# Kernel tuning notes

Measured on AMD Instinct MI355X. Metric: run time of the kernel, lower is better.

The kernel has to match this reference:

```python
import jax, jax.numpy as jnp
import numpy as np

D_MODEL = 1024
N_HEADS = 16
D_HEAD = D_MODEL // N_HEADS
WINDOW = 64
SCALE = 1.0 / np.sqrt(D_HEAD)


def setup_inputs() -> dict:
    key = jax.random.key(0)
    k1, k2, k3 = jax.random.split(key, 3)
    B, N = 1, 4096
    x = jax.random.normal(k1, (B, N, D_MODEL), dtype=jnp.float32)
    # xavier-uniform-ish init for weights (scaled normal is fine for a numeric reference)
    w_qkv = jax.random.normal(k2, (3 * D_MODEL, D_MODEL), dtype=jnp.float32) * (1.0 / np.sqrt(D_MODEL))
    b_qkv = jnp.zeros((3 * D_MODEL,), dtype=jnp.float32)
    w_out = jax.random.normal(k3, (D_MODEL, D_MODEL), dtype=jnp.float32) * (1.0 / np.sqrt(D_MODEL))
    b_out = jnp.zeros((D_MODEL,), dtype=jnp.float32)
    return {"x": x, "w_qkv": w_qkv, "b_qkv": b_qkv, "w_out": w_out, "b_out": b_out}


def reference(x, w_qkv, b_qkv, w_out, b_out):
    B, N, D = x.shape
    # QKV projection (torch Linear: x @ W^T + b)
    qkv = x @ w_qkv.T + b_qkv                      # [B, N, 3D]
    qkv = qkv.reshape(B, N, 3, N_HEADS, D_HEAD)
    qkv = jnp.transpose(qkv, (2, 0, 3, 1, 4))       # [3, B, H, N, dh]
    q, k, v = qkv[0], qkv[1], qkv[2]
    # dense scores, masked to causal sliding window (faithful to original)
    scores = jnp.einsum('bhqd,bhkd->bhqk', q, k) * SCALE  # [B, H, N, N]
    qpos = jnp.arange(N)[:, None]
    kpos = jnp.arange(N)[None, :]
    diff = qpos - kpos
    mask = (diff >= 0) & (diff < WINDOW)            # [N, N]
    scores = jnp.where(mask[None, None, :, :], scores, -jnp.inf)
    attn = jax.nn.softmax(scores, axis=-1)          # every query has >=1 valid key (self)
    out = jnp.einsum('bhqk,bhkd->bhqd', attn, v)    # [B, H, N, dh]
    out = jnp.transpose(out, (0, 2, 1, 3)).reshape(B, N, D)
    out = out @ w_out.T + b_out
    return out
```

## Files before the change

### kernel.cpp

```cpp
#include <hip/hip_runtime.h>
#include <hip/hip_bf16.h>
#include <stdint.h>
#include <stddef.h>

#define NSEQ  4096
#define DM    1024
#define NHEAD 16
#define DHEAD 64
#define WIN   64

using short8 = __attribute__((ext_vector_type(8))) short;
using f32x4  = __attribute__((ext_vector_type(4))) float;

#define GLOBAL_AS __attribute__((address_space(1)))
#define LDS_AS    __attribute__((address_space(3)))

__device__ __forceinline__ unsigned short f2bf(float f) {
  union { float f; unsigned int u; } v; v.f = f;
  unsigned int r = v.u + 0x7FFFu + ((v.u >> 16) & 1u);
  return (unsigned short)(r >> 16);
}

__device__ __forceinline__ void gload_lds16(void* lds, const void* g) {
  __builtin_amdgcn_global_load_lds((const GLOBAL_AS unsigned int*)g,
                                   (LDS_AS unsigned int*)lds, 16, 0, 0);
}

__global__ void cvt_kernel(const float* __restrict__ src,
                           unsigned short* __restrict__ dst, int n4) {
  int i = blockIdx.x * blockDim.x + threadIdx.x;
  if (i < n4) {
    float4 f = ((const float4*)src)[i];
    ushort4 o;
    o.x = f2bf(f.x); o.y = f2bf(f.y); o.z = f2bf(f.z); o.w = f2bf(f.w);
    ((ushort4*)dst)[i] = o;
  }
}

template<int EPI>
__global__ __launch_bounds__(256)
void gemm_bt(const unsigned short* __restrict__ A,
             const unsigned short* __restrict__ B,
             const float* __restrict__ bias,
             float* __restrict__ Cf,
             unsigned short* __restrict__ qo,
             unsigned short* __restrict__ ko,
             unsigned short* __restrict__ vo,
             int M, int N, int K) {
  __shared__ short As[2][128 * 32];
  __shared__ short Bs[2][128 * 32];

  const int nbn = N >> 7;
  const int bm  = blockIdx.x / nbn;
  const int bn  = blockIdx.x % nbn;
  const int tid = threadIdx.x;
  const int w   = tid >> 6;
  const int l   = tid & 63;
  const int wr  = w >> 1, wc = w & 1;
  const int l15 = l & 15, l4 = l >> 4;

  const int m0 = bm << 7;
  const int n0 = bn << 7;

  f32x4 acc[4][4] = {};

  const int nkt = K >> 5;

  auto stage = [&](int buf, int kt) {
    const int kbase = kt << 5;
#pragma unroll
    for (int r = 0; r < 2; ++r) {
      const int c   = r * 4 + w;
      const int row = c * 16 + (l >> 2);
      const int ke  = (l & 3) << 3;
      gload_lds16(&As[buf][c * 512 + l * 8],
                  A + (size_t)(m0 + row) * K + kbase + ke);
      gload_lds16(&Bs[buf][c * 512 + l * 8],
                  B + (size_t)(n0 + row) * K + kbase + ke);
    }
  };

  stage(0, 0);
  int cur = 0;
  for (int kt = 0; kt < nkt; ++kt) {
    __syncthreads();
    if (kt + 1 < nkt) stage(cur ^ 1, kt + 1);
    short8 a[4], b[4];
#pragma unroll
    for (int mi = 0; mi < 4; ++mi)
      a[mi] = *(const short8*)&As[cur][(wr * 64 + mi * 16 + l15) * 32 + l4 * 8];
#pragma unroll
    for (int ni = 0; ni < 4; ++ni)
      b[ni] = *(const short8*)&Bs[cur][(wc * 64 + ni * 16 + l15) * 32 + l4 * 8];
#pragma unroll
    for (int mi = 0; mi < 4; ++mi)
#pragma unroll
      for (int ni = 0; ni < 4; ++ni)
        acc[mi][ni] = __builtin_amdgcn_mfma_f32_16x16x32_bf16(a[mi], b[ni], acc[mi][ni], 0, 0, 0);
    cur ^= 1;
  }

  if (EPI == 0) {
#pragma unroll
    for (int ni = 0; ni < 4; ++ni) {
      const int n  = n0 + wc * 64 + ni * 16 + l15;
      const float bv = bias[n];
      const int region = n >> 10;
#pragma unroll
      for (int mi = 0; mi < 4; ++mi) {
        const int mb = m0 + wr * 64 + mi * 16 + l4 * 4;
        if (region == 0) {
          const int h = (n >> 6) & 15, d = n & 63;
#pragma unroll
          for (int r = 0; r < 4; ++r)
            qo[((size_t)(h * NSEQ + mb + r)) * DHEAD + d] =
                f2bf((acc[mi][ni][r] + bv) * 0.125f);
        } else if (region == 1) {
          const int nn = n - 1024;
          const int h = nn >> 6, d = nn & 63;
#pragma unroll
          for (int r = 0; r < 4; ++r)
            ko[((size_t)(h * NSEQ + mb + r)) * DHEAD + d] =
                f2bf(acc[mi][ni][r] + bv);
        } else {
          const int nn = n - 2048;
          ushort4 pk;
          pk.x = f2bf(acc[mi][ni][0] + bv);
          pk.y = f2bf(acc[mi][ni][1] + bv);
          pk.z = f2bf(acc[mi][ni][2] + bv);
          pk.w = f2bf(acc[mi][ni][3] + bv);
          *(ushort4*)&vo[(size_t)nn * NSEQ + mb] = pk;
        }
      }
    }
  } else {
#pragma unroll
    for (int ni = 0; ni < 4; ++ni) {
      const int n  = n0 + wc * 64 + ni * 16 + l15;
      const float bv = bias[n];
#pragma unroll
      for (int mi = 0; mi < 4; ++mi) {
        const int mb = m0 + wr * 64 + mi * 16 + l4 * 4;
#pragma unroll
        for (int r = 0; r < 4; ++r)
          Cf[(size_t)(mb + r) * N + n] = acc[mi][ni][r] + bv;
      }
    }
  }
}

__global__ __launch_bounds__(256)
void attn_kernel(const unsigned short* __restrict__ Qb,
                 const unsigned short* __restrict__ Kb,
                 const unsigned short* __restrict__ Vt,
                 unsigned short* __restrict__ att) {
  __shared__ short Pl[4][16][136];
  const int h  = blockIdx.x >> 6;
  const int q0 = (blockIdx.x & 63) << 6;
  const int w  = threadIdx.x >> 6;
  const int l  = threadIdx.x & 63;
  const int l15 = l & 15, l4 = l >> 4;
  const int qw = q0 + w * 16;

  const unsigned short* Qh = Qb + (size_t)h * NSEQ * DHEAD;
  const unsigned short* Kh = Kb + (size_t)h * NSEQ * DHEAD;
  const unsigned short* Vh = Vt + (size_t)h * DHEAD * NSEQ;

  short8 aq[2];
  {
    const int qrow = qw + l15;
    aq[0] = *(const short8*)&Qh[(size_t)qrow * DHEAD + l4 * 8];
    aq[1] = *(const short8*)&Qh[(size_t)qrow * DHEAD + 32 + l4 * 8];
  }

  f32x4 s[8] = {};
#pragma unroll
  for (int t = 0; t < 8; ++t) {
    int j  = q0 - 64 + t * 16 + l15;
    int jc = j < 0 ? 0 : j;
    short8 b0 = *(const short8*)&Kh[(size_t)jc * DHEAD + l4 * 8];
    short8 b1 = *(const short8*)&Kh[(size_t)jc * DHEAD + 32 + l4 * 8];
    s[t] = __builtin_amdgcn_mfma_f32_16x16x32_bf16(aq[0], b0, s[t], 0, 0, 0);
    s[t] = __builtin_amdgcn_mfma_f32_16x16x32_bf16(aq[1], b1, s[t], 0, 0, 0);
  }

  float rmax[4] = {-3e38f, -3e38f, -3e38f, -3e38f};
#pragma unroll
  for (int t = 0; t < 8; ++t)
#pragma unroll
    for (int r = 0; r < 4; ++r) {
      const int i = qw + l4 * 4 + r;
      const int j = q0 - 64 + t * 16 + l15;
      const int diff = i - j;
      float sv = (j >= 0 && diff >= 0 && diff < WIN) ? s[t][r] : -3e38f;
      s[t][r] = sv;
      rmax[r] = fmaxf(rmax[r], sv);
    }
#pragma unroll
  for (int r = 0; r < 4; ++r)
#pragma unroll
    for (int m = 1; m < 16; m <<= 1)
      rmax[r] = fmaxf(rmax[r], __shfl_xor(rmax[r], m, 64));

  float rsum[4] = {0.f, 0.f, 0.f, 0.f};
#pragma unroll
  for (int t = 0; t < 8; ++t)
#pragma unroll
    for (int r = 0; r < 4; ++r) {
      float p = __expf(s[t][r] - rmax[r]);
      s[t][r] = p;
      rsum[r] += p;
    }
#pragma unroll
  for (int r = 0; r < 4; ++r)
#pragma unroll
    for (int m = 1; m < 16; m <<= 1)
      rsum[r] += __shfl_xor(rsum[r], m, 64);

#pragma unroll
  for (int t = 0; t < 8; ++t)
#pragma unroll
    for (int r = 0; r < 4; ++r)
      Pl[w][l4 * 4 + r][t * 16 + l15] = (short)f2bf(s[t][r]);

  f32x4 o[4] = {};
#pragma unroll
  for (int ks = 0; ks < 4; ++ks) {
    short8 ap = *(const short8*)&Pl[w][l15][ks * 32 + l4 * 8];
    int jg = q0 - 64 + ks * 32 + l4 * 8;
    if (jg < 0) jg = 0;
#pragma unroll
    for (int dt = 0; dt < 4; ++dt) {
      const int d = dt * 16 + l15;
      short8 bv = *(const short8*)&Vh[(size_t)d * NSEQ + jg];
      o[dt] = __builtin_amdgcn_mfma_f32_16x16x32_bf16(ap, bv, o[dt], 0, 0, 0);
    }
  }

#pragma unroll
  for (int r = 0; r < 4; ++r) {
    const float rinv = 1.0f / rsum[r];
    const int m = qw + l4 * 4 + r;
#pragma unroll
    for (int dt = 0; dt < 4; ++dt)
      att[(size_t)m * DM + h * DHEAD + dt * 16 + l15] = f2bf(o[dt][r] * rinv);
  }
}

extern "C" void kernel_launch(void* const* d_in, const int* in_sizes, int n_in,
                              void* d_out, int out_size, void* d_ws, size_t ws_size,
                              hipStream_t stream) {
  const float* x    = (const float*)d_in[0];
  const float* wqkv = (const float*)d_in[1];
  const float* bqkv = (const float*)d_in[2];
  const float* wout = (const float*)d_in[3];
  const float* bout = (const float*)d_in[4];
  float* out = (float*)d_out;

  unsigned short* ws = (unsigned short*)d_ws;
  unsigned short* xb    = ws;
  unsigned short* wqkvb = xb    + (size_t)NSEQ * DM;
  unsigned short* woutb = wqkvb + (size_t)3 * DM * DM;
  unsigned short* qb    = woutb + (size_t)DM * DM;
  unsigned short* kb    = qb    + (size_t)NSEQ * DM;
  unsigned short* vtb   = kb    + (size_t)NSEQ * DM;
  unsigned short* attb  = vtb   + (size_t)NSEQ * DM;

  cvt_kernel<<<(NSEQ * DM / 4 + 255) / 256, 256, 0, stream>>>(x, xb, NSEQ * DM / 4);
  cvt_kernel<<<(3 * DM * DM / 4 + 255) / 256, 256, 0, stream>>>(wqkv, wqkvb, 3 * DM * DM / 4);
  cvt_kernel<<<(DM * DM / 4 + 255) / 256, 256, 0, stream>>>(wout, woutb, DM * DM / 4);

  gemm_bt<0><<<(NSEQ / 128) * (3 * DM / 128), 256, 0, stream>>>(
      xb, wqkvb, bqkv, nullptr, qb, kb, vtb, NSEQ, 3 * DM, DM);

  attn_kernel<<<NHEAD * (NSEQ / 64), 256, 0, stream>>>(qb, kb, vtb, attb);

  gemm_bt<1><<<(NSEQ / 128) * (DM / 128), 256, 0, stream>>>(
      attb, woutb, bout, out, nullptr, nullptr, nullptr, NSEQ, DM, DM);
}
```

Before: 98.05 us.

## Replace QKV projection GEMM with 256x256-tile 8-wave triple-buffered kernel

Adds a dedicated QKV projection kernel using 256x256 output tiles, 512 threads (8 waves), a three-stage LDS ring buffer with XOR-swizzled layout, explicit vmcnt waits and barriers, and setprio around the MFMA blocks. The larger tile gives more reuse per loaded byte, and the deeper pipeline overlaps global-to-LDS loads with compute. The trade-off is that the grid shrinks to 192 blocks, fewer than the number of CUs, and register pressure rises with 32 accumulators per lane. The generic GEMM template is reduced to the output-projection path only.

```diff
diff --git a/kernel.cpp b/kernel.cpp
--- a/kernel.cpp
+++ b/kernel.cpp
@@ -8,6 +8,7 @@
 #define NHEAD 16
 #define DHEAD 64
 #define WIN   64
+#define K_QKV 1024
 
 using short8 = __attribute__((ext_vector_type(8))) short;
 using f32x4  = __attribute__((ext_vector_type(4))) float;
@@ -37,15 +38,123 @@
   }
 }
 
-template<int EPI>
+__global__ __launch_bounds__(512, 2)
+void gemm_qkv8(const unsigned short* __restrict__ A,
+               const unsigned short* __restrict__ B,
+               const float* __restrict__ bias,
+               unsigned short* __restrict__ qo,
+               unsigned short* __restrict__ ko,
+               unsigned short* __restrict__ vo) {
+  __shared__ short lds[12 * 4096];
+
+  const int bm = blockIdx.x / 12;
+  const int bn = blockIdx.x % 12;
+  const int m0 = bm << 8, n0 = bn << 8;
+  const int tid = threadIdx.x, w = tid >> 6, l = tid & 63;
+  const int wr = w >> 2, wc = w & 3;
+  const int l15 = l & 15, l4 = l >> 4;
+
+  const int srow = (w << 4) + (l >> 2);
+  const int skel = ((l & 3) << 3) ^ ((l >= 32) << 4);
+  const int sdst = (w << 9) + (l << 3);
+
+  f32x4 acc[8][4] = {};
+
+  auto stage = [&](int s, int slot) {
+    const int h = s & 3, t = s >> 2;
+    const unsigned short* src;
+    if (h < 2) src = A + (size_t)(m0 + (h << 7) + srow) * K_QKV + (t << 5) + skel;
+    else       src = B + (size_t)(n0 + ((h & 1) << 7) + srow) * K_QKV + (t << 5) + skel;
+    gload_lds16(&lds[slot * 4096 + sdst], src);
+  };
+
+#pragma unroll
+  for (int s = 0; s < 8; ++s) stage(s, s);
+  asm volatile("s_waitcnt vmcnt(4)" ::: "memory");
+  asm volatile("s_barrier" ::: "memory");
+
+  const int NT = K_QKV / 32;
+  int bufC = 0;
+  for (int t = 0; t < NT; ++t) {
+    const int sbase = 4 * t + 8;
+    const int slotb = (bufC == 0 ? 2 : bufC - 1) * 4;
+    const short* At = &lds[(bufC * 4 + wr) * 4096];
+    const short* Bt = &lds[(bufC * 4 + 2 + (wc >> 1)) * 4096];
+    const int bn0 = (wc & 1) << 6;
+    short8 af[4], bf[2];
+#pragma unroll
+    for (int q = 0; q < 4; ++q) {
+      const int qa = q >> 1, qb = q & 1;
+      if (qb == 0) {
+#pragma unroll
+        for (int mi = 0; mi < 4; ++mi) {
+          const int sr = qa * 4 + mi;
+          af[mi] = *(const short8*)&At[sr * 512 + l15 * 32 + ((l4 * 8) ^ ((l15 >= 8) * 16))];
+        }
+      }
+#pragma unroll
+      for (int ni = 0; ni < 2; ++ni) {
+        const int sr = (bn0 >> 4) + qb * 2 + ni;
+        bf[ni] = *(const short8*)&Bt[sr * 512 + l15 * 32 + ((l4 * 8) ^ ((l15 >= 8) * 16))];
+      }
+      if (t < NT - 2) stage(sbase + q, slotb + q);
+      if (q == 3) {
+        if (t < NT - 2)      asm volatile("s_waitcnt vmcnt(4)" ::: "memory");
+        else if (t == NT - 2) asm volatile("s_waitcnt vmcnt(0)" ::: "memory");
+      }
+      asm volatile("s_barrier" ::: "memory");
+      __builtin_amdgcn_s_setprio(1);
+#pragma unroll
+      for (int mi = 0; mi < 4; ++mi)
+#pragma unroll
+        for (int ni = 0; ni < 2; ++ni)
+          acc[qa * 4 + mi][qb * 2 + ni] = __builtin_amdgcn_mfma_f32_16x16x32_bf16(
+              af[mi], bf[ni], acc[qa * 4 + mi][qb * 2 + ni], 0, 0, 0);
+      __builtin_amdgcn_s_setprio(0);
+      asm volatile("s_barrier" ::: "memory");
+    }
+    bufC = bufC == 2 ? 0 : bufC + 1;
+  }
+
+#pragma unroll
+  for (int ni = 0; ni < 4; ++ni) {
+    const int gn = n0 + wc * 64 + ni * 16 + l15;
+    const float bv = bias[gn];
+    const int region = gn >> 10;
+#pragma unroll
+    for (int mi = 0; mi < 8; ++mi) {
+      const int gm = m0 + wr * 128 + mi * 16 + l4 * 4;
+      if (region == 0) {
+        const int h = (gn >> 6) & 15, d = gn & 63;
+#pragma unroll
+        for (int r = 0; r < 4; ++r)
+          qo[((size_t)(h * NSEQ + gm + r)) * DHEAD + d] =
+              f2bf((acc[mi][ni][r] + bv) * 0.125f);
+      } else if (region == 1) {
+        const int nn = gn - 1024;
+        const int h = nn >> 6, d = nn & 63;
+#pragma unroll
+        for (int r = 0; r < 4; ++r)
+          ko[((size_t)(h * NSEQ + gm + r)) * DHEAD + d] =
+              f2bf(acc[mi][ni][r] + bv);
+      } else {
+        const int nn = gn - 2048;
+        ushort4 pk;
+        pk.x = f2bf(acc[mi][ni][0] + bv);
+        pk.y = f2bf(acc[mi][ni][1] + bv);
+        pk.z = f2bf(acc[mi][ni][2] + bv);
+        pk.w = f2bf(acc[mi][ni][3] + bv);
+        *(ushort4*)&vo[(size_t)nn * NSEQ + gm] = pk;
+      }
+    }
+  }
+}
+
 __global__ __launch_bounds__(256)
 void gemm_bt(const unsigned short* __restrict__ A,
              const unsigned short* __restrict__ B,
              const float* __restrict__ bias,
              float* __restrict__ Cf,
-             unsigned short* __restrict__ qo,
-             unsigned short* __restrict__ ko,
-             unsigned short* __restrict__ vo,
              int M, int N, int K) {
   __shared__ short As[2][128 * 32];
   __shared__ short Bs[2][128 * 32];
@@ -63,7 +172,6 @@
   const int n0 = bn << 7;
 
   f32x4 acc[4][4] = {};
-
   const int nkt = K >> 5;
 
   auto stage = [&](int buf, int kt) {
@@ -100,51 +208,16 @@
     cur ^= 1;
   }
 
-  if (EPI == 0) {
-#pragma unroll
-    for (int ni = 0; ni < 4; ++ni) {
-      const int n  = n0 + wc * 64 + ni * 16 + l15;
-      const float bv = bias[n];
-      const int region = n >> 10;
-#pragma unroll
-      for (int mi = 0; mi < 4; ++mi) {
-        const int mb = m0 + wr * 64 + mi * 16 + l4 * 4;
-        if (region == 0) {
-          const int h = (n >> 6) & 15, d = n & 63;
-#pragma unroll
-          for (int r = 0; r < 4; ++r)
-            qo[((size_t)(h * NSEQ + mb + r)) * DHEAD + d] =
-                f2bf((acc[mi][ni][r] + bv) * 0.125f);
-        } else if (region == 1) {
-          const int nn = n - 1024;
-          const int h = nn >> 6, d = nn & 63;
-#pragma unroll
-          for (int r = 0; r < 4; ++r)
-            ko[((size_t)(h * NSEQ + mb + r)) * DHEAD + d] =
-                f2bf(acc[mi][ni][r] + bv);
-        } else {
-          const int nn = n - 2048;
-          ushort4 pk;
-          pk.x = f2bf(acc[mi][ni][0] + bv);
-          pk.y = f2bf(acc[mi][ni][1] + bv);
-          pk.z = f2bf(acc[mi][ni][2] + bv);
-          pk.w = f2bf(acc[mi][ni][3] + bv);
-          *(ushort4*)&vo[(size_t)nn * NSEQ + mb] = pk;
-        }
-      }
-    }
-  } else {
-#pragma unroll
-    for (int ni = 0; ni < 4; ++ni) {
-      const int n  = n0 + wc * 64 + ni * 16 + l15;
-      const float bv = bias[n];
-#pragma unroll
-      for (int mi = 0; mi < 4; ++mi) {
-        const int mb = m0 + wr * 64 + mi * 16 + l4 * 4;
-#pragma unroll
-        for (int r = 0; r < 4; ++r)
-          Cf[(size_t)(mb + r) * N + n] = acc[mi][ni][r] + bv;
-      }
+#pragma unroll
+  for (int ni = 0; ni < 4; ++ni) {
+    const int n  = n0 + wc * 64 + ni * 16 + l15;
+    const float bv = bias[n];
+#pragma unroll
+    for (int mi = 0; mi < 4; ++mi) {
+      const int mb = m0 + wr * 64 + mi * 16 + l4 * 4;
+#pragma unroll
+      for (int r = 0; r < 4; ++r)
+        Cf[(size_t)(mb + r) * N + n] = acc[mi][ni][r] + bv;
     }
   }
 }
@@ -270,11 +343,11 @@
   cvt_kernel<<<(3 * DM * DM / 4 + 255) / 256, 256, 0, stream>>>(wqkv, wqkvb, 3 * DM * DM / 4);
   cvt_kernel<<<(DM * DM / 4 + 255) / 256, 256, 0, stream>>>(wout, woutb, DM * DM / 4);
 
-  gemm_bt<0><<<(NSEQ / 128) * (3 * DM / 128), 256, 0, stream>>>(
-      xb, wqkvb, bqkv, nullptr, qb, kb, vtb, NSEQ, 3 * DM, DM);
+  gemm_qkv8<<<(NSEQ / 256) * (3 * DM / 256), 512, 0, stream>>>(
+      xb, wqkvb, bqkv, qb, kb, vtb);
 
   attn_kernel<<<NHEAD * (NSEQ / 64), 256, 0, stream>>>(qb, kb, vtb, attb);
 
-  gemm_bt<1><<<(NSEQ / 128) * (DM / 128), 256, 0, stream>>>(
-      attb, woutb, bout, out, nullptr, nullptr, nullptr, NSEQ, DM, DM);
-}
+  gemm_bt<<<(NSEQ / 128) * (DM / 128), 256, 0, stream>>>(
+      attb, woutb, bout, out, NSEQ, DM, DM);
+}
```

Result: slower. 101.0 us (+3.0%).

## Triple-buffer GEMM with swizzled LDS, fine-grained waitcnt, and fused conversion kernel

Applied to the files above, without the earlier changes.

The three fp32-to-bf16 conversion launches are merged into one kernel that writes into the contiguous workspace. The GEMM moves from double to triple buffering with prefetch two tiles ahead. It uses explicit vmcnt waits and a raw s_barrier in place of __syncthreads, and raises wave priority around the MFMA block. LDS addressing gets an XOR swizzle to cut bank conflicts on fragment reads. The cost is more LDS per block and hand-managed synchronisation, which is fragile if the load counts change.

```diff
diff --git a/kernel.cpp b/kernel.cpp
--- a/kernel.cpp
+++ b/kernel.cpp
@@ -26,78 +26,88 @@
                                    (LDS_AS unsigned int*)lds, 16, 0, 0);
 }
 
-__global__ void cvt_kernel(const float* __restrict__ src,
-                           unsigned short* __restrict__ dst, int n4) {
+#define NX4 1048576
+#define NW4 786432
+__global__ void cvt_all(const float* __restrict__ x,
+                        const float* __restrict__ wqkv,
+                        const float* __restrict__ wout,
+                        unsigned short* __restrict__ dst) {
   int i = blockIdx.x * blockDim.x + threadIdx.x;
-  if (i < n4) {
-    float4 f = ((const float4*)src)[i];
-    ushort4 o;
-    o.x = f2bf(f.x); o.y = f2bf(f.y); o.z = f2bf(f.z); o.w = f2bf(f.w);
-    ((ushort4*)dst)[i] = o;
-  }
+  float4 f;
+  if (i < NX4)            f = ((const float4*)x)[i];
+  else if (i < NX4 + NW4) f = ((const float4*)wqkv)[i - NX4];
+  else                    f = ((const float4*)wout)[i - (NX4 + NW4)];
+  ushort4 o;
+  o.x = f2bf(f.x); o.y = f2bf(f.y); o.z = f2bf(f.z); o.w = f2bf(f.w);
+  ((ushort4*)dst)[i] = o;
 }
 
 template<int EPI>
 __global__ __launch_bounds__(256)
-void gemm_bt(const unsigned short* __restrict__ A,
-             const unsigned short* __restrict__ B,
-             const float* __restrict__ bias,
-             float* __restrict__ Cf,
-             unsigned short* __restrict__ qo,
-             unsigned short* __restrict__ ko,
-             unsigned short* __restrict__ vo,
-             int M, int N, int K) {
-  __shared__ short As[2][128 * 32];
-  __shared__ short Bs[2][128 * 32];
+void gemm3(const unsigned short* __restrict__ A,
+           const unsigned short* __restrict__ B,
+           const float* __restrict__ bias,
+           float* __restrict__ Cf,
+           unsigned short* __restrict__ qo,
+           unsigned short* __restrict__ ko,
+           unsigned short* __restrict__ vo,
+           int M, int N, int K) {
+  __shared__ short lds[3][8192];
 
   const int nbn = N >> 7;
   const int bm  = blockIdx.x / nbn;
   const int bn  = blockIdx.x % nbn;
-  const int tid = threadIdx.x;
-  const int w   = tid >> 6;
-  const int l   = tid & 63;
+  const int m0  = bm << 7, n0 = bn << 7;
+  const int tid = threadIdx.x, w = tid >> 6, l = tid & 63;
   const int wr  = w >> 1, wc = w & 1;
   const int l15 = l & 15, l4 = l >> 4;
 
-  const int m0 = bm << 7;
-  const int n0 = bn << 7;
+  const int skel = ((l & 3) << 3) ^ ((l >= 32) << 4);
+  const int roff = l15 * 32 + ((l4 * 8) ^ ((l15 >= 8) * 16));
 
   f32x4 acc[4][4] = {};
-
-  const int nkt = K >> 5;
-
-  auto stage = [&](int buf, int kt) {
-    const int kbase = kt << 5;
+  const int NT = K >> 5;
+
+  auto stage = [&](int t) {
+    const int buf = t % 3;
+    const int kb  = t << 5;
 #pragma unroll
     for (int r = 0; r < 2; ++r) {
       const int c   = r * 4 + w;
       const int row = c * 16 + (l >> 2);
-      const int ke  = (l & 3) << 3;
-      gload_lds16(&As[buf][c * 512 + l * 8],
-                  A + (size_t)(m0 + row) * K + kbase + ke);
-      gload_lds16(&Bs[buf][c * 512 + l * 8],
-                  B + (size_t)(n0 + row) * K + kbase + ke);
+      gload_lds16(&lds[buf][c * 512 + l * 8],
+                  A + (size_t)(m0 + row) * K + kb + skel);
+      gload_lds16(&lds[buf][4096 + c * 512 + l * 8],
+                  B + (size_t)(n0 + row) * K + kb + skel);
     }
   };
 
-  stage(0, 0);
-  int cur = 0;
-  for (int kt = 0; kt < nkt; ++kt) {
-    __syncthreads();
-    if (kt + 1 < nkt) stage(cur ^ 1, kt + 1);
-    short8 a[4], b[4];
+  stage(0);
+  stage(1);
+  asm volatile("s_waitcnt vmcnt(4)" ::: "memory");
+  __builtin_amdgcn_s_barrier();
+
+  for (int t = 0; t < NT; ++t) {
+    const short* Ab = &lds[t % 3][0];
+    const short* Bb = &lds[t % 3][4096];
+    short8 af[4], bf[4];
+#pragma unroll
+    for (int i = 0; i < 4; ++i) {
+      af[i] = *(const short8*)&Ab[(wr * 4 + i) * 512 + roff];
+      bf[i] = *(const short8*)&Bb[(wc * 4 + i) * 512 + roff];
+    }
+    if (t + 2 < NT) stage(t + 2);
+    if (t + 2 < NT)       asm volatile("s_waitcnt vmcnt(4)" ::: "memory");
+    else if (t + 2 == NT) asm volatile("s_waitcnt vmcnt(0)" ::: "memory");
+    __builtin_amdgcn_s_barrier();
+    __builtin_amdgcn_s_setprio(1);
 #pragma unroll
     for (int mi = 0; mi < 4; ++mi)
-      a[mi] = *(const short8*)&As[cur][(wr * 64 + mi * 16 + l15) * 32 + l4 * 8];
-#pragma unroll
-    for (int ni = 0; ni < 4; ++ni)
-      b[ni] = *(const short8*)&Bs[cur][(wc * 64 + ni * 16 + l15) * 32 + l4 * 8];
-#pragma unroll
-    for (int mi = 0; mi < 4; ++mi)
 #pragma unroll
       for (int ni = 0; ni < 4; ++ni)
-        acc[mi][ni] = __builtin_amdgcn_mfma_f32_16x16x32_bf16(a[mi], b[ni], acc[mi][ni], 0, 0, 0);
-    cur ^= 1;
+        acc[mi][ni] = __builtin_amdgcn_mfma_f32_16x16x32_bf16(
+            af[mi], bf[ni], acc[mi][ni], 0, 0, 0);
+    __builtin_amdgcn_s_setprio(0);
   }
 
   if (EPI == 0) {
@@ -266,15 +276,13 @@
   unsigned short* vtb   = kb    + (size_t)NSEQ * DM;
   unsigned short* attb  = vtb   + (size_t)NSEQ * DM;
 
-  cvt_kernel<<<(NSEQ * DM / 4 + 255) / 256, 256, 0, stream>>>(x, xb, NSEQ * DM / 4);
-  cvt_kernel<<<(3 * DM * DM / 4 + 255) / 256, 256, 0, stream>>>(wqkv, wqkvb, 3 * DM * DM / 4);
-  cvt_kernel<<<(DM * DM / 4 + 255) / 256, 256, 0, stream>>>(wout, woutb, DM * DM / 4);
-
-  gemm_bt<0><<<(NSEQ / 128) * (3 * DM / 128), 256, 0, stream>>>(
+  cvt_all<<<8192, 256, 0, stream>>>(x, wqkv, wout, xb);
+
+  gemm3<0><<<(NSEQ / 128) * (3 * DM / 128), 256, 0, stream>>>(
       xb, wqkvb, bqkv, nullptr, qb, kb, vtb, NSEQ, 3 * DM, DM);
 
   attn_kernel<<<NHEAD * (NSEQ / 64), 256, 0, stream>>>(qb, kb, vtb, attb);
 
-  gemm_bt<1><<<(NSEQ / 128) * (DM / 128), 256, 0, stream>>>(
+  gemm3<1><<<(NSEQ / 128) * (DM / 128), 256, 0, stream>>>(
       attb, woutb, bout, out, nullptr, nullptr, nullptr, NSEQ, DM, DM);
 }
```

Result: faster. 89.58 us (-8.6%).
